# Kernel tuning notes

Hardware: AMD Instinct MI355X
Metric: run time of the kernel (lower is better)

## Reference

```python
import jax, jax.numpy as jnp
import numpy as np

N_NODES = 50000
N_EDGES = 1600000
N_INPUT = 256
HID = 32
OUT = N_INPUT // 2
EPS = 1e-12


def gcn_conv(x, edge_index, W, b):
    # Standard GCNConv: D^{-1/2} (A + I) D^{-1/2} X W + b
    N = x.shape[0]
    loop = jnp.arange(N)
    src = jnp.concatenate([edge_index[0], loop])
    dst = jnp.concatenate([edge_index[1], loop])
    deg = jax.ops.segment_sum(jnp.ones_like(src, dtype=x.dtype), dst, num_segments=N)
    dinv = jax.lax.rsqrt(jnp.maximum(deg, 1.0))  # deg >= 1 due to self-loops
    norm = dinv[src] * dinv[dst]                  # [E+N]
    h = x @ W                                     # [N, out]
    msg = h[src] * norm[:, None]                  # gather + scale
    out = jax.ops.segment_sum(msg, dst, num_segments=N)
    return out + b


def l2_normalize(z):
    n = jnp.linalg.norm(z, axis=1, keepdims=True)
    return z / jnp.maximum(n, EPS)


def setup_inputs() -> dict:
    key = jax.random.key(0)
    ks = jax.random.split(key, 9)
    x = jax.random.normal(ks[0], (N_NODES, N_INPUT), dtype=jnp.float32)
    ei_u = jax.random.randint(ks[1], (2, N_EDGES), 0, N_NODES)
    ei_u2 = jax.random.randint(ks[2], (2, N_EDGES), 0, N_NODES)
    s_in = 1.0 / np.sqrt(N_INPUT)
    s_hid = 1.0 / np.sqrt(HID)
    W_in = jax.random.normal(ks[3], (N_INPUT, HID), dtype=jnp.float32) * s_in
    b_in = jnp.zeros((HID,), dtype=jnp.float32)
    W_hid = jax.random.normal(ks[4], (HID, HID), dtype=jnp.float32) * s_hid
    b_hid = jnp.zeros((HID,), dtype=jnp.float32)
    W_out = jax.random.normal(ks[5], (HID, OUT), dtype=jnp.float32) * s_hid
    b_out = jnp.zeros((OUT,), dtype=jnp.float32)
    return {"x": x, "edge_index_u": ei_u, "edge_index_u2": ei_u2,
            "W_in": W_in, "b_in": b_in, "W_hid": W_hid, "b_hid": b_hid,
            "W_out": W_out, "b_out": b_out}


def reference(x, edge_index_u, edge_index_u2, W_in, b_in, W_hid, b_hid, W_out, b_out):
    # layer 1 on both views
    x1 = gcn_conv(x, edge_index_u, W_in, b_in)
    x2 = gcn_conv(x, edge_index_u2, W_in, b_in)
    sim = jnp.sum(l2_normalize(x1) * l2_normalize(x2), axis=1, keepdims=True)
    mian = x1 + x2 * sim
    sup = x2 + x1 * sim
    # layer 2
    x1 = gcn_conv(mian, edge_index_u, W_hid, b_hid)
    x2 = gcn_conv(sup, edge_index_u2, W_hid, b_hid)
    sim = jnp.sum(l2_normalize(x1) * l2_normalize(x2), axis=1, keepdims=True)
    mian = x1 + x2 * sim
    sup = x2 + x1 * sim
    # layer 3: note both branches use edge_index_u (as in source)
    x1 = gcn_conv(mian, edge_index_u, W_out, b_out)
    x2 = gcn_conv(sup, edge_index_u, W_out, b_out)
    return jnp.concatenate([x1, x2], axis=1)
```

## Files before the change

### kernel.cpp

```cpp
#include <hip/hip_runtime.h>
#include <hip/hip_bf16.h>

#define NN 50000
#define NE 1600000
#define NIN 256
#define HID 32
#define FOUT 128
#define OSTR 256
#define NSB ((NN + 255) / 256)
#define CHUNK 4096
#define NCH ((NE + CHUNK - 1) / CHUNK)

static constexpr float EPS = 1e-12f;

__device__ __forceinline__ float b2f(unsigned short s) {
    return __uint_as_float((unsigned)s << 16);
}
__device__ __forceinline__ unsigned short f2b(float f) {
    unsigned u = __float_as_uint(f);
    u += 0x7FFFu + ((u >> 16) & 1u);
    return (unsigned short)(u >> 16);
}
__device__ __forceinline__ unsigned pack2(float a, float b) {
    return (unsigned)f2b(a) | ((unsigned)f2b(b) << 16);
}

__global__ __launch_bounds__(256) void k_hist(const int* __restrict__ dstA,
                                              const int* __restrict__ dstB,
                                              unsigned* __restrict__ hcA,
                                              unsigned* __restrict__ hcB, int half) {
    __shared__ unsigned h[NSB];
    for (int i = threadIdx.x; i < NSB; i += 256) h[i] = 0u;
    __syncthreads();
    bool sec = blockIdx.x >= half;
    int c = sec ? blockIdx.x - half : blockIdx.x;
    const int* dst = sec ? dstB : dstA;
    unsigned* hc = sec ? hcB : hcA;
    int beg = c * CHUNK, end = min(beg + CHUNK, NE);
    for (int e = beg + (int)threadIdx.x; e < end; e += 256)
        atomicAdd(&h[dst[e] >> 8], 1u);
    __syncthreads();
    for (int i = threadIdx.x; i < NSB; i += 256) hc[(size_t)c * NSB + i] = h[i];
}

__global__ __launch_bounds__(256) void k_cscan(unsigned* __restrict__ hcA,
                                               unsigned* __restrict__ hcB,
                                               unsigned* __restrict__ totA,
                                               unsigned* __restrict__ totB, int half) {
    __shared__ unsigned tile[256];
    __shared__ unsigned carry;
    bool sec = blockIdx.x >= half;
    int sb = sec ? blockIdx.x - half : blockIdx.x;
    unsigned* hc = sec ? hcB : hcA;
    unsigned* tot = sec ? totB : totA;
    if (threadIdx.x == 0) carry = 0u;
    __syncthreads();
    for (int base = 0; base < NCH; base += 256) {
        int c = base + (int)threadIdx.x;
        unsigned v = (c < NCH) ? hc[(size_t)c * NSB + sb] : 0u;
        tile[threadIdx.x] = v;
        __syncthreads();
        for (int off = 1; off < 256; off <<= 1) {
            unsigned t = (threadIdx.x >= (unsigned)off) ? tile[threadIdx.x - off] : 0u;
            __syncthreads();
            tile[threadIdx.x] += t;
            __syncthreads();
        }
        if (c < NCH) hc[(size_t)c * NSB + sb] = carry + tile[threadIdx.x] - v;
        __syncthreads();
        if (threadIdx.x == 0) carry += tile[255];
        __syncthreads();
    }
    if (threadIdx.x == 0) tot[sb] = carry;
}

__global__ __launch_bounds__(256) void k_bscan(const unsigned* __restrict__ totA,
                                               const unsigned* __restrict__ totB,
                                               int* __restrict__ bbA, int* __restrict__ bbB) {
    __shared__ unsigned tile[256];
    const unsigned* tot = blockIdx.x ? totB : totA;
    int* bb = blockIdx.x ? bbB : bbA;
    unsigned v = (threadIdx.x < NSB) ? tot[threadIdx.x] : 0u;
    tile[threadIdx.x] = v;
    __syncthreads();
    for (int off = 1; off < 256; off <<= 1) {
        unsigned t = (threadIdx.x >= (unsigned)off) ? tile[threadIdx.x - off] : 0u;
        __syncthreads();
        tile[threadIdx.x] += t;
        __syncthreads();
    }
    if (threadIdx.x < NSB) bb[threadIdx.x] = (int)(tile[threadIdx.x] - v);
    if (threadIdx.x == 0) bb[NSB] = NE;
}

__global__ __launch_bounds__(256) void k_bin1(const int* __restrict__ srcA,
                                              const int* __restrict__ dstA,
                                              const unsigned* __restrict__ hcA,
                                              const int* __restrict__ bbA,
                                              int* __restrict__ tmpA,
                                              const int* __restrict__ srcB,
                                              const int* __restrict__ dstB,
                                              const unsigned* __restrict__ hcB,
                                              const int* __restrict__ bbB,
                                              int* __restrict__ tmpB, int half) {
    __shared__ unsigned hbase[NSB];
    __shared__ unsigned hcur[NSB];
    __shared__ unsigned hscan[NSB];
    __shared__ unsigned tile[256];
    __shared__ unsigned pay[CHUNK];
    __shared__ unsigned gpos[CHUNK];
    bool sec = blockIdx.x >= half;
    int c = sec ? blockIdx.x - half : blockIdx.x;
    const int* src = sec ? srcB : srcA;
    const int* dst = sec ? dstB : dstA;
    const unsigned* hc = sec ? hcB : hcA;
    const int* bb = sec ? bbB : bbA;
    int* tmp = sec ? tmpB : tmpA;
    for (int i = threadIdx.x; i < NSB; i += 256) {
        hbase[i] = (unsigned)bb[i] + hc[(size_t)c * NSB + i];
        hcur[i] = 0u;
    }
    __syncthreads();
    int beg = c * CHUNK;
    int len = min(CHUNK, NE - beg);
    int d[16], s[16];
#pragma unroll
    for (int j = 0; j < 16; ++j) {
        int idx = j * 256 + (int)threadIdx.x;
        if (idx < len) { d[j] = dst[beg + idx]; s[j] = src[beg + idx]; }
        else d[j] = -1;
    }
#pragma unroll
    for (int j = 0; j < 16; ++j)
        if (d[j] >= 0) atomicAdd(&hcur[d[j] >> 8], 1u);
    __syncthreads();
    unsigned v = (threadIdx.x < NSB) ? hcur[threadIdx.x] : 0u;
    tile[threadIdx.x] = v;
    __syncthreads();
    for (int off = 1; off < 256; off <<= 1) {
        unsigned t = (threadIdx.x >= (unsigned)off) ? tile[threadIdx.x - off] : 0u;
        __syncthreads();
        tile[threadIdx.x] += t;
        __syncthreads();
    }
    if (threadIdx.x < NSB) {
        unsigned excl = tile[threadIdx.x] - v;
        hscan[threadIdx.x] = excl;
        hcur[threadIdx.x] = excl;
    }
    __syncthreads();
#pragma unroll
    for (int j = 0; j < 16; ++j) {
        if (d[j] >= 0) {
            int sb = d[j] >> 8;
            unsigned p = atomicAdd(&hcur[sb], 1u);
            pay[p] = ((unsigned)(d[j] & 255) << 16) | (unsigned)s[j];
            gpos[p] = hbase[sb] + (p - hscan[sb]);
        }
    }
    __syncthreads();
    for (int i = threadIdx.x; i < len; i += 256)
        tmp[gpos[i]] = (int)pay[i];
}

__global__ __launch_bounds__(256) void k_bin2(const int* __restrict__ tmpA,
                                              const int* __restrict__ bbA,
                                              unsigned short* __restrict__ csrA,
                                              unsigned* __restrict__ degA,
                                              float* __restrict__ dinvA,
                                              int* __restrict__ rpA,
                                              const int* __restrict__ tmpB,
                                              const int* __restrict__ bbB,
                                              unsigned short* __restrict__ csrB,
                                              unsigned* __restrict__ degB,
                                              float* __restrict__ dinvB,
                                              int* __restrict__ rpB, int half) {
    __shared__ unsigned cnt[256];
    __shared__ unsigned scan[256];
    __shared__ unsigned curs[256];
    bool sec = blockIdx.x >= half;
    int sb = sec ? blockIdx.x - half : blockIdx.x;
    const int* tmp = sec ? tmpB : tmpA;
    const int* bb = sec ? bbB : bbA;
    unsigned short* csr = sec ? csrB : csrA;
    unsigned* deg = sec ? degB : degA;
    float* dinv = sec ? dinvB : dinvA;
    int* rp = sec ? rpB : rpA;
    int beg = bb[sb], end = bb[sb + 1];
    cnt[threadIdx.x] = 0u;
    __syncthreads();
    for (int e = beg + (int)threadIdx.x; e < end; e += 256)
        atomicAdd(&cnt[(tmp[e] >> 16) & 255], 1u);
    __syncthreads();
    unsigned v = cnt[threadIdx.x];
    scan[threadIdx.x] = v;
    __syncthreads();
    for (int off = 1; off < 256; off <<= 1) {
        unsigned t = (threadIdx.x >= (unsigned)off) ? scan[threadIdx.x - off] : 0u;
        __syncthreads();
        scan[threadIdx.x] += t;
        __syncthreads();
    }
    unsigned excl = scan[threadIdx.x] - v;
    int n = sb * 256 + (int)threadIdx.x;
    if (n < NN) {
        deg[n] = v;
        rp[n] = beg + (int)excl;
        dinv[n] = rsqrtf((float)(v + 1u));
    }
    curs[threadIdx.x] = (unsigned)beg + excl;
    __syncthreads();
    for (int e = beg + (int)threadIdx.x; e < end; e += 256) {
        int p = tmp[e];
        unsigned pos = atomicAdd(&curs[(p >> 16) & 255], 1u);
        csr[pos] = (unsigned short)(p & 0xFFFF);
    }
}

__global__ __launch_bounds__(256) void k_gemm_in(const float* __restrict__ x,
                                                 const float* __restrict__ W,
                                                 const float* __restrict__ dinvU,
                                                 const float* __restrict__ dinvV,
                                                 unsigned short* __restrict__ hU,
                                                 unsigned short* __restrict__ hV, int N) {
    __shared__ float part[4 * 64 * 33];
    int lane = threadIdx.x & 63;
    int wv = __builtin_amdgcn_readfirstlane((int)(threadIdx.x >> 6));
    int row = blockIdx.x * 64 + lane;
    float acc[32];
#pragma unroll
    for (int j = 0; j < 32; ++j) acc[j] = 0.f;
    if (row < N) {
        const float4* xr = reinterpret_cast<const float4*>(x + (size_t)row * NIN);
#pragma unroll 4
        for (int i = 0; i < 16; ++i) {
            int k4 = wv * 16 + i;
            float4 v = xr[k4];
            const float* Wk = W + k4 * 4 * HID;
#pragma unroll
            for (int j = 0; j < 32; ++j) {
                acc[j] = fmaf(v.x, Wk[j], acc[j]);
                acc[j] = fmaf(v.y, Wk[HID + j], acc[j]);
                acc[j] = fmaf(v.z, Wk[2 * HID + j], acc[j]);
                acc[j] = fmaf(v.w, Wk[3 * HID + j], acc[j]);
            }
        }
    }
    float* pw = part + (wv * 64 + lane) * 33;
#pragma unroll
    for (int j = 0; j < 32; ++j) pw[j] = acc[j];
    __syncthreads();
    int r = threadIdx.x >> 2;
    int c0 = (threadIdx.x & 3) * 8;
    int orow = blockIdx.x * 64 + r;
    if (orow >= N) return;
    float s[8];
#pragma unroll
    for (int i = 0; i < 8; ++i) {
        s[i] = part[(0 * 64 + r) * 33 + c0 + i]
             + part[(1 * 64 + r) * 33 + c0 + i]
             + part[(2 * 64 + r) * 33 + c0 + i]
             + part[(3 * 64 + r) * 33 + c0 + i];
    }
    float du = dinvU[orow], dw = dinvV[orow];
    uint4 wu, wvv;
    wu.x = pack2(s[0] * du, s[1] * du); wu.y = pack2(s[2] * du, s[3] * du);
    wu.z = pack2(s[4] * du, s[5] * du); wu.w = pack2(s[6] * du, s[7] * du);
    wvv.x = pack2(s[0] * dw, s[1] * dw); wvv.y = pack2(s[2] * dw, s[3] * dw);
    wvv.z = pack2(s[4] * dw, s[5] * dw); wvv.w = pack2(s[6] * dw, s[7] * dw);
    *reinterpret_cast<uint4*>(hU + (size_t)orow * HID + c0) = wu;
    *reinterpret_cast<uint4*>(hV + (size_t)orow * HID + c0) = wvv;
}

__device__ __forceinline__ void pull_sum(const unsigned short* __restrict__ t,
                                         const unsigned short* __restrict__ csr,
                                         const int* __restrict__ rowptr,
                                         const unsigned* __restrict__ deg,
                                         float* __restrict__ out, int blk, int tid) {
    int node = blk * 32 + tid / 8;
    int q = tid % 8;
    if (node >= NN) return;
    const ushort4* h4 = reinterpret_cast<const ushort4*>(t);
    int beg = rowptr[node];
    int end = beg + (int)deg[node];
    ushort4 sv = h4[(size_t)node * 8 + q];
    float4 acc0, acc1;
    acc0.x = b2f(sv.x); acc0.y = b2f(sv.y); acc0.z = b2f(sv.z); acc0.w = b2f(sv.w);
    acc1.x = 0.f; acc1.y = 0.f; acc1.z = 0.f; acc1.w = 0.f;
    int e = beg;
    for (; e + 8 <= end; e += 8) {
        int s0 = csr[e],     s1 = csr[e + 1], s2 = csr[e + 2], s3 = csr[e + 3];
        int s4 = csr[e + 4], s5 = csr[e + 5], s6 = csr[e + 6], s7 = csr[e + 7];
        ushort4 v0 = h4[(size_t)s0 * 8 + q];
        ushort4 v1 = h4[(size_t)s1 * 8 + q];
        ushort4 v2 = h4[(size_t)s2 * 8 + q];
        ushort4 v3 = h4[(size_t)s3 * 8 + q];
        ushort4 v4 = h4[(size_t)s4 * 8 + q];
        ushort4 v5 = h4[(size_t)s5 * 8 + q];
        ushort4 v6 = h4[(size_t)s6 * 8 + q];
        ushort4 v7 = h4[(size_t)s7 * 8 + q];
        acc0.x += (b2f(v0.x) + b2f(v1.x)) + (b2f(v2.x) + b2f(v3.x));
        acc0.y += (b2f(v0.y) + b2f(v1.y)) + (b2f(v2.y) + b2f(v3.y));
        acc0.z += (b2f(v0.z) + b2f(v1.z)) + (b2f(v2.z) + b2f(v3.z));
        acc0.w += (b2f(v0.w) + b2f(v1.w)) + (b2f(v2.w) + b2f(v3.w));
        acc1.x += (b2f(v4.x) + b2f(v5.x)) + (b2f(v6.x) + b2f(v7.x));
        acc1.y += (b2f(v4.y) + b2f(v5.y)) + (b2f(v6.y) + b2f(v7.y));
        acc1.z += (b2f(v4.z) + b2f(v5.z)) + (b2f(v6.z) + b2f(v7.z));
        acc1.w += (b2f(v4.w) + b2f(v5.w)) + (b2f(v6.w) + b2f(v7.w));
    }
    if (e + 4 <= end) {
        int s0 = csr[e], s1 = csr[e + 1], s2 = csr[e + 2], s3 = csr[e + 3];
        ushort4 v0 = h4[(size_t)s0 * 8 + q];
        ushort4 v1 = h4[(size_t)s1 * 8 + q];
        ushort4 v2 = h4[(size_t)s2 * 8 + q];
        ushort4 v3 = h4[(size_t)s3 * 8 + q];
        acc1.x += (b2f(v0.x) + b2f(v1.x)) + (b2f(v2.x) + b2f(v3.x));
        acc1.y += (b2f(v0.y) + b2f(v1.y)) + (b2f(v2.y) + b2f(v3.y));
        acc1.z += (b2f(v0.z) + b2f(v1.z)) + (b2f(v2.z) + b2f(v3.z));
        acc1.w += (b2f(v0.w) + b2f(v1.w)) + (b2f(v2.w) + b2f(v3.w));
        e += 4;
    }
    for (; e < end; ++e) {
        ushort4 v0 = h4[(size_t)csr[e] * 8 + q];
        acc0.x += b2f(v0.x); acc0.y += b2f(v0.y);
        acc0.z += b2f(v0.z); acc0.w += b2f(v0.w);
    }
    float4 acc;
    acc.x = acc0.x + acc1.x; acc.y = acc0.y + acc1.y;
    acc.z = acc0.z + acc1.z; acc.w = acc0.w + acc1.w;
    *reinterpret_cast<float4*>(out + (size_t)node * HID + q * 4) = acc;
}

__global__ __launch_bounds__(256) void k_pull_pair(
    const unsigned short* __restrict__ tA, const unsigned short* __restrict__ csrA,
    const int* __restrict__ rpA, const unsigned* __restrict__ degA, float* __restrict__ outA,
    const unsigned short* __restrict__ tB, const unsigned short* __restrict__ csrB,
    const int* __restrict__ rpB, const unsigned* __restrict__ degB, float* __restrict__ outB,
    int nblk) {
    int b = blockIdx.x;
    int xcd = b & 7;
    int blk = (b >> 3) * 4 + (xcd & 3);
    if (blk >= nblk) return;
    if (xcd >= 4) pull_sum(tB, csrB, rpB, degB, outB, blk, threadIdx.x);
    else          pull_sum(tA, csrA, rpA, degA, outA, blk, threadIdx.x);
}

__global__ __launch_bounds__(256) void k_mix1(const float* __restrict__ Su,
                                              const float* __restrict__ Sv,
                                              const float* __restrict__ dinvU,
                                              const float* __restrict__ dinvV,
                                              const float* __restrict__ bias,
                                              unsigned short* __restrict__ Tu,
                                              unsigned short* __restrict__ Tv) {
    int node = blockIdx.x * 32 + (threadIdx.x >> 3);
    int q = threadIdx.x & 7;
    if (node >= NN) return;
    float4 su = *reinterpret_cast<const float4*>(Su + (size_t)node * HID + 4 * q);
    float4 sv = *reinterpret_cast<const float4*>(Sv + (size_t)node * HID + 4 * q);
    float du = dinvU[node], dw = dinvV[node];
    float a0 = fmaf(su.x, du, bias[4 * q + 0]);
    float a1 = fmaf(su.y, du, bias[4 * q + 1]);
    float a2 = fmaf(su.z, du, bias[4 * q + 2]);
    float a3 = fmaf(su.w, du, bias[4 * q + 3]);
    float b0 = fmaf(sv.x, dw, bias[4 * q + 0]);
    float b1 = fmaf(sv.y, dw, bias[4 * q + 1]);
    float b2 = fmaf(sv.z, dw, bias[4 * q + 2]);
    float b3 = fmaf(sv.w, dw, bias[4 * q + 3]);
    float n1 = a0 * a0 + a1 * a1 + a2 * a2 + a3 * a3;
    float n2 = b0 * b0 + b1 * b1 + b2 * b2 + b3 * b3;
    float dt = a0 * b0 + a1 * b1 + a2 * b2 + a3 * b3;
#pragma unroll
    for (int m = 4; m >= 1; m >>= 1) {
        n1 += __shfl_xor(n1, m);
        n2 += __shfl_xor(n2, m);
        dt += __shfl_xor(dt, m);
    }
    float sim = dt / (fmaxf(sqrtf(n1), EPS) * fmaxf(sqrtf(n2), EPS));
    uint2 mu, mv;
    mu.x = pack2((a0 + b0 * sim) * du, (a1 + b1 * sim) * du);
    mu.y = pack2((a2 + b2 * sim) * du, (a3 + b3 * sim) * du);
    mv.x = pack2((b0 + a0 * sim) * dw, (b1 + a1 * sim) * dw);
    mv.y = pack2((b2 + a2 * sim) * dw, (b3 + a3 * sim) * dw);
    *reinterpret_cast<uint2*>(Tu + (size_t)node * HID + 4 * q) = mu;
    *reinterpret_cast<uint2*>(Tv + (size_t)node * HID + 4 * q) = mv;
}

__global__ __launch_bounds__(256) void k_hid_mix_pack(const float* __restrict__ Su,
                                                      const float* __restrict__ Sv,
                                                      const float* __restrict__ W,
                                                      const float* __restrict__ bias,
                                                      const float* __restrict__ dinvU,
                                                      const float* __restrict__ dinvV,
                                                      unsigned short* __restrict__ Pa,
                                                      unsigned short* __restrict__ Pb) {
    __shared__ float Ws[HID * HID];
    __shared__ float zu[32][33];
    __shared__ float zv[32][33];
    int t = threadIdx.x;
    for (int i = t; i < HID * HID; i += 256) Ws[i] = W[i];
    int nb = blockIdx.x * 32;
    int l = t >> 3, q = t & 7;
    int node = nb + l;
    {
        float4 fu = make_float4(0.f, 0.f, 0.f, 0.f), fv = fu;
        if (node < NN) {
            fu = *reinterpret_cast<const float4*>(Su + (size_t)node * HID + 4 * q);
            fv = *reinterpret_cast<const float4*>(Sv + (size_t)node * HID + 4 * q);
        }
        zu[l][4 * q + 0] = fu.x; zu[l][4 * q + 1] = fu.y;
        zu[l][4 * q + 2] = fu.z; zu[l][4 * q + 3] = fu.w;
        zv[l][4 * q + 0] = fv.x; zv[l][4 * q + 1] = fv.y;
        zv[l][4 * q + 2] = fv.z; zv[l][4 * q + 3] = fv.w;
    }
    __syncthreads();
    if (node >= NN) return;
    float a[4] = {0.f, 0.f, 0.f, 0.f};
    float b[4] = {0.f, 0.f, 0.f, 0.f};
#pragma unroll
    for (int k = 0; k < HID; ++k) {
        float zuk = zu[l][k], zvk = zv[l][k];
        const float* Wk = Ws + k * HID + 4 * q;
#pragma unroll
        for (int j = 0; j < 4; ++j) {
            a[j] = fmaf(zuk, Wk[j], a[j]);
            b[j] = fmaf(zvk, Wk[j], b[j]);
        }
    }
    float du = dinvU[node], dw = dinvV[node];
#pragma unroll
    for (int j = 0; j < 4; ++j) {
        a[j] = fmaf(a[j], du, bias[4 * q + j]);
        b[j] = fmaf(b[j], dw, bias[4 * q + j]);
    }
    float n1 = a[0]*a[0] + a[1]*a[1] + a[2]*a[2] + a[3]*a[3];
    float n2 = b[0]*b[0] + b[1]*b[1] + b[2]*b[2] + b[3]*b[3];
    float dt = a[0]*b[0] + a[1]*b[1] + a[2]*b[2] + a[3]*b[3];
#pragma unroll
    for (int m = 4; m >= 1; m >>= 1) {
        n1 += __shfl_xor(n1, m);
        n2 += __shfl_xor(n2, m);
        dt += __shfl_xor(dt, m);
    }
    float sim = dt / (fmaxf(sqrtf(n1), EPS) * fmaxf(sqrtf(n2), EPS));
    uint2 ma, mb;
    ma.x = pack2((a[0] + b[0] * sim) * du, (a[1] + b[1] * sim) * du);
    ma.y = pack2((a[2] + b[2] * sim) * du, (a[3] + b[3] * sim) * du);
    mb.x = pack2((b[0] + a[0] * sim) * du, (b[1] + a[1] * sim) * du);
    mb.y = pack2((b[2] + a[2] * sim) * du, (b[3] + a[3] * sim) * du);
    *reinterpret_cast<uint2*>(Pa + (size_t)node * HID + 4 * q) = ma;
    *reinterpret_cast<uint2*>(Pb + (size_t)node * HID + 4 * q) = mb;
}

__global__ __launch_bounds__(512) void k_gemm_out2(const float* __restrict__ Qa,
                                                   const float* __restrict__ Qb,
                                                   const float* __restrict__ dinvU,
                                                   const float* __restrict__ W,
                                                   const float* __restrict__ b,
                                                   float* __restrict__ out, int N) {
    __shared__ float ob[32 * 257];
    int lane = threadIdx.x & 63;
    int wv = (int)(threadIdx.x >> 6);
    int view = __builtin_amdgcn_readfirstlane(wv >> 2);
    int c0 = __builtin_amdgcn_readfirstlane((wv & 3) * 32);
    int row = blockIdx.x * 64 + lane;
    bool active = row < N;
    float a[32];
#pragma unroll
    for (int j = 0; j < 32; ++j) a[j] = 0.f;
    if (active) {
        const float* Q = view ? Qb : Qa;
        const float4* q4 = reinterpret_cast<const float4*>(Q + (size_t)row * HID);
#pragma unroll 2
        for (int k4 = 0; k4 < 8; ++k4) {
            float4 v = q4[k4];
            const float* Wk = W + (k4 * 4) * FOUT + c0;
#pragma unroll
            for (int j = 0; j < 32; ++j) {
                a[j] = fmaf(v.x, Wk[j], a[j]);
                a[j] = fmaf(v.y, Wk[FOUT + j], a[j]);
                a[j] = fmaf(v.z, Wk[2 * FOUT + j], a[j]);
                a[j] = fmaf(v.w, Wk[3 * FOUT + j], a[j]);
            }
        }
    }
    float du = active ? dinvU[row] : 0.f;
    int r32 = lane & 31;
    int hl = lane >> 5;
    for (int p = 0; p < 2; ++p) {
        if (hl == p) {
            int off = r32 * 257 + view * FOUT + c0;
#pragma unroll
            for (int j = 0; j < 32; ++j)
                ob[off + j] = fmaf(a[j], du, b[c0 + j]);
        }
        __syncthreads();
        int rbase = blockIdx.x * 64 + p * 32;
        int nrows = min(32, N - rbase);
        if (nrows > 0) {
            float* obase = out + (size_t)rbase * OSTR;
            int total = nrows * OSTR;
            for (int f = threadIdx.x; f < total; f += 512)
                obase[f] = ob[f + (f >> 8)];
        }
        __syncthreads();
    }
}

extern "C" void kernel_launch(void* const* d_in, const int* in_sizes, int n_in,
                              void* d_out, int out_size, void* d_ws, size_t ws_size,
                              hipStream_t stream) {
    const float* x     = (const float*)d_in[0];
    const int*   ei_u  = (const int*)d_in[1];
    const int*   ei_u2 = (const int*)d_in[2];
    const float* W_in  = (const float*)d_in[3];
    const float* b_in  = (const float*)d_in[4];
    const float* W_hid = (const float*)d_in[5];
    const float* b_hid = (const float*)d_in[6];
    const float* W_out = (const float*)d_in[7];
    const float* b_out = (const float*)d_in[8];
    float* out = (float*)d_out;

    const int* src_u  = ei_u;
    const int* dst_u  = ei_u + NE;
    const int* src_u2 = ei_u2;
    const int* dst_u2 = ei_u2 + NE;

    char* w = (char*)d_ws;
    auto carve = [&](size_t bytes) {
        char* p = w;
        w += (bytes + 255) & ~(size_t)255;
        return p;
    };
    unsigned* hc_u   = (unsigned*)carve((size_t)NCH * NSB * sizeof(unsigned));
    unsigned* hc_u2  = (unsigned*)carve((size_t)NCH * NSB * sizeof(unsigned));
    unsigned* tot_u  = (unsigned*)carve(NSB * sizeof(unsigned));
    unsigned* tot_u2 = (unsigned*)carve(NSB * sizeof(unsigned));
    int*      bb_u   = (int*)carve((NSB + 1) * sizeof(int));
    int*      bb_u2  = (int*)carve((NSB + 1) * sizeof(int));
    unsigned* deg_u  = (unsigned*)carve(NN * sizeof(unsigned));
    unsigned* deg_u2 = (unsigned*)carve(NN * sizeof(unsigned));
    float*    dinv_u  = (float*)carve(NN * sizeof(float));
    float*    dinv_u2 = (float*)carve(NN * sizeof(float));
    int*      rp_u   = (int*)carve(NN * sizeof(int));
    int*      rp_u2  = (int*)carve(NN * sizeof(int));
    unsigned short* csr_u  = (unsigned short*)carve((size_t)NE * sizeof(unsigned short));
    unsigned short* csr_u2 = (unsigned short*)carve((size_t)NE * sizeof(unsigned short));
    unsigned short* hU = (unsigned short*)carve((size_t)NN * HID * sizeof(unsigned short));
    unsigned short* hV = (unsigned short*)carve((size_t)NN * HID * sizeof(unsigned short));
    unsigned short* Tu = (unsigned short*)carve((size_t)NN * HID * sizeof(unsigned short));
    unsigned short* Tv = (unsigned short*)carve((size_t)NN * HID * sizeof(unsigned short));
    unsigned short* Pa = (unsigned short*)carve((size_t)NN * HID * sizeof(unsigned short));
    unsigned short* Pb = (unsigned short*)carve((size_t)NN * HID * sizeof(unsigned short));
    float* Su = (float*)carve((size_t)NN * HID * sizeof(float));
    float* Sv = (float*)carve((size_t)NN * HID * sizeof(float));
    int* tmp_u  = (int*)Su;
    int* tmp_u2 = (int*)Sv;

    const int BLK = 256;
    const int gP32 = (NN + 31) / 32;
    const int nPair = ((gP32 + 3) / 4) * 8;
    const int gR64 = (NN + 63) / 64;

    k_hist<<<2 * NCH, BLK, 0, stream>>>(dst_u, dst_u2, hc_u, hc_u2, NCH);
    k_cscan<<<2 * NSB, BLK, 0, stream>>>(hc_u, hc_u2, tot_u, tot_u2, NSB);
    k_bscan<<<2, BLK, 0, stream>>>(tot_u, tot_u2, bb_u, bb_u2);
    k_bin1<<<2 * NCH, BLK, 0, stream>>>(src_u, dst_u, hc_u, bb_u, tmp_u,
                                        src_u2, dst_u2, hc_u2, bb_u2, tmp_u2, NCH);
    k_bin2<<<2 * NSB, BLK, 0, stream>>>(tmp_u, bb_u, csr_u, deg_u, dinv_u, rp_u,
                                        tmp_u2, bb_u2, csr_u2, deg_u2, dinv_u2, rp_u2, NSB);

    k_gemm_in<<<gR64, BLK, 0, stream>>>(x, W_in, dinv_u, dinv_u2, hU, hV, NN);
    k_pull_pair<<<nPair, BLK, 0, stream>>>(hU, csr_u, rp_u, deg_u, Su,
                                           hV, csr_u2, rp_u2, deg_u2, Sv, gP32);
    k_mix1<<<gP32, BLK, 0, stream>>>(Su, Sv, dinv_u, dinv_u2, b_in, Tu, Tv);

    k_pull_pair<<<nPair, BLK, 0, stream>>>(Tu, csr_u, rp_u, deg_u, Su,
                                           Tv, csr_u2, rp_u2, deg_u2, Sv, gP32);
    k_hid_mix_pack<<<gP32, BLK, 0, stream>>>(Su, Sv, W_hid, b_hid, dinv_u, dinv_u2, Pa, Pb);

    k_pull_pair<<<nPair, BLK, 0, stream>>>(Pa, csr_u, rp_u, deg_u, Su,
                                           Pb, csr_u, rp_u, deg_u, Sv, gP32);
    k_gemm_out2<<<gR64, 512, 0, stream>>>(Su, Sv, dinv_u, W_out, b_out, out, NN);

    (void)in_sizes; (void)n_in; (void)out_size; (void)ws_size;
}
```

Baseline: 198.2 us.

## Stage x tiles in shared memory and split input GEMM by output columns

The input projection kernel used to split the K dimension across four waves, each lane loading its own strided row of x, and then reduced the partial sums through shared memory. It now loads 64x64 tiles of x cooperatively with coalesced float4 reads, stores them transposed in padded shared memory, and has each wave compute 8 output columns over the full K range. This removes the cross-wave reduction and the uncoalesced per-row global reads, and cuts accumulator registers from 32 to 8. In exchange it adds four tile loads with two barriers each.

```diff
diff --git a/kernel.cpp b/kernel.cpp
--- a/kernel.cpp
+++ b/kernel.cpp
@@ -223,53 +223,52 @@
                                                  const float* __restrict__ dinvV,
                                                  unsigned short* __restrict__ hU,
                                                  unsigned short* __restrict__ hV, int N) {
-    __shared__ float part[4 * 64 * 33];
-    int lane = threadIdx.x & 63;
-    int wv = __builtin_amdgcn_readfirstlane((int)(threadIdx.x >> 6));
-    int row = blockIdx.x * 64 + lane;
-    float acc[32];
-#pragma unroll
-    for (int j = 0; j < 32; ++j) acc[j] = 0.f;
-    if (row < N) {
-        const float4* xr = reinterpret_cast<const float4*>(x + (size_t)row * NIN);
-#pragma unroll 4
-        for (int i = 0; i < 16; ++i) {
-            int k4 = wv * 16 + i;
-            float4 v = xr[k4];
-            const float* Wk = W + k4 * 4 * HID;
-#pragma unroll
-            for (int j = 0; j < 32; ++j) {
-                acc[j] = fmaf(v.x, Wk[j], acc[j]);
-                acc[j] = fmaf(v.y, Wk[HID + j], acc[j]);
-                acc[j] = fmaf(v.z, Wk[2 * HID + j], acc[j]);
-                acc[j] = fmaf(v.w, Wk[3 * HID + j], acc[j]);
-            }
-        }
-    }
-    float* pw = part + (wv * 64 + lane) * 33;
-#pragma unroll
-    for (int j = 0; j < 32; ++j) pw[j] = acc[j];
-    __syncthreads();
-    int r = threadIdx.x >> 2;
-    int c0 = (threadIdx.x & 3) * 8;
-    int orow = blockIdx.x * 64 + r;
-    if (orow >= N) return;
-    float s[8];
-#pragma unroll
-    for (int i = 0; i < 8; ++i) {
-        s[i] = part[(0 * 64 + r) * 33 + c0 + i]
-             + part[(1 * 64 + r) * 33 + c0 + i]
-             + part[(2 * 64 + r) * 33 + c0 + i]
-             + part[(3 * 64 + r) * 33 + c0 + i];
-    }
-    float du = dinvU[orow], dw = dinvV[orow];
+    __shared__ float xs[64][65];
+    int t = threadIdx.x;
+    int lane = t & 63;
+    int c0 = __builtin_amdgcn_readfirstlane((t >> 6) * 8);
+    int rbase = blockIdx.x * 64;
+    int row = rbase + lane;
+    float acc[8];
+#pragma unroll
+    for (int j = 0; j < 8; ++j) acc[j] = 0.f;
+    int sr = t >> 2;
+    int so = (t & 3) * 4;
+    int grow = rbase + sr;
+    const float* xrow = x + (size_t)grow * NIN;
+    for (int kt = 0; kt < 4; ++kt) {
+        int k0 = kt * 64;
+        __syncthreads();
+#pragma unroll
+        for (int p = 0; p < 4; ++p) {
+            int ko = so + p * 16;
+            float4 v = make_float4(0.f, 0.f, 0.f, 0.f);
+            if (grow < N) v = *reinterpret_cast<const float4*>(xrow + k0 + ko);
+            xs[ko + 0][sr] = v.x;
+            xs[ko + 1][sr] = v.y;
+            xs[ko + 2][sr] = v.z;
+            xs[ko + 3][sr] = v.w;
+        }
+        __syncthreads();
+        const float* Wk = W + k0 * HID + c0;
+#pragma unroll 8
+        for (int k = 0; k < 64; ++k) {
+            float xv = xs[k][lane];
+            const float* Wr = Wk + k * HID;
+#pragma unroll
+            for (int j = 0; j < 8; ++j)
+                acc[j] = fmaf(xv, Wr[j], acc[j]);
+        }
+    }
+    if (row >= N) return;
+    float du = dinvU[row], dw = dinvV[row];
     uint4 wu, wvv;
-    wu.x = pack2(s[0] * du, s[1] * du); wu.y = pack2(s[2] * du, s[3] * du);
-    wu.z = pack2(s[4] * du, s[5] * du); wu.w = pack2(s[6] * du, s[7] * du);
-    wvv.x = pack2(s[0] * dw, s[1] * dw); wvv.y = pack2(s[2] * dw, s[3] * dw);
-    wvv.z = pack2(s[4] * dw, s[5] * dw); wvv.w = pack2(s[6] * dw, s[7] * dw);
-    *reinterpret_cast<uint4*>(hU + (size_t)orow * HID + c0) = wu;
-    *reinterpret_cast<uint4*>(hV + (size_t)orow * HID + c0) = wvv;
+    wu.x = pack2(acc[0] * du, acc[1] * du); wu.y = pack2(acc[2] * du, acc[3] * du);
+    wu.z = pack2(acc[4] * du, acc[5] * du); wu.w = pack2(acc[6] * du, acc[7] * du);
+    wvv.x = pack2(acc[0] * dw, acc[1] * dw); wvv.y = pack2(acc[2] * dw, acc[3] * dw);
+    wvv.z = pack2(acc[4] * dw, acc[5] * dw); wvv.w = pack2(acc[6] * dw, acc[7] * dw);
+    *reinterpret_cast<uint4*>(hU + (size_t)row * HID + c0) = wu;
+    *reinterpret_cast<uint4*>(hV + (size_t)row * HID + c0) = wvv;
 }
 
 __device__ __forceinline__ void pull_sum(const unsigned short* __restrict__ t,
```

After: 204.1 us. 3.0% more time.
